# Kernel tuning notes

Hardware: AMD Instinct MI355X
Metric: run time of the kernel (lower is better)

The kernel has to match this reference:

```python
import jax, jax.numpy as jnp
import numpy as np

D_MODEL = 512
D_STATE = 64
D_CONV = 4
D_INNER = 1024   # expand=2 * d_model (mamba_ssm default)
DT_RANK = 32     # ceil(d_model/16)
NUM_CLASSES = 8
B, T, P, F = 8, 250, 20, 24   # x: [B, T*P=5000, F=24]
FLAT = T * P * F              # 120000 = fc1 input dim


def _mamba(u, in_proj_w, conv_w, conv_b, x_proj_w, dt_proj_w, dt_proj_b, A_log, D, out_proj_w):
    # u: [b, L, d_model]
    b, L, _ = u.shape
    xz = jnp.einsum('bld,ed->ble', u, in_proj_w)      # [b, L, 2*d_inner]
    x, z = jnp.split(xz, 2, axis=-1)                  # each [b, L, d_inner]
    # depthwise causal conv1d, kernel width D_CONV, truncated to L
    x_pad = jnp.pad(x, ((0, 0), (D_CONV - 1, 0), (0, 0)))
    x = sum(x_pad[:, k:k + L, :] * conv_w[:, k] for k in range(D_CONV)) + conv_b
    x = jax.nn.silu(x)
    x_dbl = jnp.einsum('bld,ed->ble', x, x_proj_w)    # [b, L, dt_rank + 2*d_state]
    dt, Bm, Cm = jnp.split(x_dbl, [DT_RANK, DT_RANK + D_STATE], axis=-1)
    dt = jax.nn.softplus(jnp.einsum('blr,dr->bld', dt, dt_proj_w) + dt_proj_b)  # [b, L, d_inner]
    A = -jnp.exp(A_log)                               # [d_inner, d_state]

    def step(h, inp):
        dt_t, B_t, C_t, u_t = inp                     # [b,d_in], [b,d_st], [b,d_st], [b,d_in]
        dA = jnp.exp(dt_t[:, :, None] * A)            # [b, d_in, d_st]
        dBu = dt_t[:, :, None] * B_t[:, None, :] * u_t[:, :, None]
        h = h * dA + dBu
        y = jnp.einsum('bds,bs->bd', h, C_t)
        return h, y

    xs = (jnp.swapaxes(dt, 0, 1), jnp.swapaxes(Bm, 0, 1), jnp.swapaxes(Cm, 0, 1), jnp.swapaxes(x, 0, 1))
    h0 = jnp.zeros((b, D_INNER, D_STATE), dtype=u.dtype)
    _, ys = jax.lax.scan(step, h0, xs)                # ys: [L, b, d_inner]
    y = jnp.swapaxes(ys, 0, 1) + x * D
    y = y * jax.nn.silu(z)
    return jnp.einsum('bld,ed->ble', y, out_proj_w)   # [b, L, d_model]


def setup_inputs() -> dict:
    key = jax.random.key(0)
    ks = jax.random.split(key, 16)
    n = lambda k, shape, s=0.02: jax.random.normal(k, shape, jnp.float32) * s
    return {
        'x': jax.random.normal(ks[0], (B, T * P, F), jnp.float32),
        'in_proj_w': n(ks[1], (2 * D_INNER, D_MODEL)),
        'conv_w': n(ks[2], (D_INNER, D_CONV), 0.1),
        'conv_b': jnp.zeros((D_INNER,), jnp.float32),
        'x_proj_w': n(ks[3], (DT_RANK + 2 * D_STATE, D_INNER)),
        'dt_proj_w': n(ks[4], (D_INNER, DT_RANK), 0.1),
        'dt_proj_b': jnp.full((D_INNER,), -4.6, jnp.float32),  # softplus -> dt ~ 0.01
        'A_log': jnp.log(jnp.broadcast_to(jnp.arange(1, D_STATE + 1, dtype=jnp.float32), (D_INNER, D_STATE))),
        'D': jnp.ones((D_INNER,), jnp.float32),
        'out_proj_w': n(ks[5], (D_MODEL, D_INNER)),
        'fc1_w': n(ks[6], (512, FLAT), 0.003),
        'fc1_b': jnp.zeros((512,), jnp.float32),
        'fc2_w': n(ks[7], (256, 512)),
        'fc2_b': jnp.zeros((256,), jnp.float32),
        'fc3_w': n(ks[8], (64, 256)),
        'fc3_b': jnp.zeros((64,), jnp.float32),
        'fc4_w': n(ks[9], (NUM_CLASSES, 64)),
        'fc4_b': jnp.zeros((NUM_CLASSES,), jnp.float32),
    }


def reference(x, in_proj_w, conv_w, conv_b, x_proj_w, dt_proj_w, dt_proj_b, A_log, D, out_proj_w,
              fc1_w, fc1_b, fc2_w, fc2_b, fc3_w, fc3_b, fc4_w, fc4_b):
    b = x.shape[0]
    u = x.reshape(b, T, P * F)                                   # [b,250,480]
    u = jnp.pad(u, ((0, 0), (0, 0), (0, D_MODEL - P * F)))       # pad 480 -> 512
    y = _mamba(u, in_proj_w, conv_w, conv_b, x_proj_w, dt_proj_w, dt_proj_b, A_log, D, out_proj_w)
    y = jax.nn.selu(y)                                           # AlphaDropout: identity in eval
    y = y[..., :P * F].reshape(b, T * P, F)                      # [b,5000,24]
    y = jnp.swapaxes(y, 1, 2).reshape(b, -1)                     # [b, 24*5000]
    y = y @ fc1_w.T + fc1_b
    y = y @ fc2_w.T + fc2_b
    y = y @ fc3_w.T + fc3_b
    return y @ fc4_w.T + fc4_b
```

## Files before the change

### kernel.cpp

```cpp
#include <hip/hip_runtime.h>
#include <math.h>

#define T_ 250
#define BL 2000
#define KIN 480
#define NFLAT 120000

typedef __attribute__((ext_vector_type(8))) short short8;
typedef __attribute__((ext_vector_type(4))) float f32x4;

__device__ __forceinline__ float sigmoidf_(float x){ return 1.0f/(1.0f+expf(-x)); }
__device__ __forceinline__ float siluf_(float x){ return x*sigmoidf_(x); }
__device__ __forceinline__ float softplusf_(float x){ return (x > 20.0f) ? x : log1pf(expf(x)); }
__device__ __forceinline__ float seluf_(float x){
  const float sc = 1.0507009873554804934193349852946f;
  const float al = 1.6732632423543772848170429916717f;
  return x > 0.0f ? sc*x : sc*al*expm1f(x);
}
__device__ __forceinline__ unsigned f2bf(float f){
  unsigned u = __builtin_bit_cast(unsigned, f);
  return (u + 0x7FFFu + ((u >> 16) & 1u)) >> 16;
}

template<int CTRL>
__device__ __forceinline__ float dpp_add(float x) {
  int t = __builtin_amdgcn_update_dpp(0, __builtin_bit_cast(int, x), CTRL, 0xF, 0xF, true);
  return x + __builtin_bit_cast(float, t);
}

__global__ __launch_bounds__(256) void inproj_mfma(
    const float* __restrict__ x, const float* __restrict__ w,
    float* __restrict__ C)
{
  __shared__ __align__(16) unsigned short As[128 * 40];
  __shared__ __align__(16) unsigned short Bs[128 * 40];
  const int tid = threadIdx.x;
  const int m0 = blockIdx.y * 128;
  const int n0 = blockIdx.x * 128;
  const int wid = tid >> 6, lane = tid & 63;
  const int wr = wid >> 1, wc = wid & 1;
  const int sr = tid >> 1;
  const int sk = (tid & 1) * 16;
  const int fr = lane & 15, fg = lane >> 4;

  float4 pa[4], pb[4];
  auto fetch = [&](int k0) {
    int m = m0 + sr;
    if (m < BL) {
      const float* xp = x + (size_t)m * KIN + k0 + sk;
      pa[0] = *(const float4*)(xp);
      pa[1] = *(const float4*)(xp + 4);
      pa[2] = *(const float4*)(xp + 8);
      pa[3] = *(const float4*)(xp + 12);
    } else {
      pa[0] = pa[1] = pa[2] = pa[3] = make_float4(0.f, 0.f, 0.f, 0.f);
    }
    const float* wp = w + (size_t)(n0 + sr) * 512 + k0 + sk;
    pb[0] = *(const float4*)(wp);
    pb[1] = *(const float4*)(wp + 4);
    pb[2] = *(const float4*)(wp + 8);
    pb[3] = *(const float4*)(wp + 12);
  };
  auto pack2 = [](float a, float b) {
    return f2bf(a) | (f2bf(b) << 16);
  };
  auto stash = [&](unsigned short* S, float4* p) {
    uint4 lo = make_uint4(pack2(p[0].x, p[0].y), pack2(p[0].z, p[0].w),
                          pack2(p[1].x, p[1].y), pack2(p[1].z, p[1].w));
    uint4 hi = make_uint4(pack2(p[2].x, p[2].y), pack2(p[2].z, p[2].w),
                          pack2(p[3].x, p[3].y), pack2(p[3].z, p[3].w));
    *(uint4*)&S[sr * 40 + sk] = lo;
    *(uint4*)&S[sr * 40 + sk + 8] = hi;
  };

  f32x4 acc[4][4];
#pragma unroll
  for (int i = 0; i < 4; ++i)
#pragma unroll
    for (int j = 0; j < 4; ++j) acc[i][j] = (f32x4)(0.0f);

  fetch(0);
  for (int k0 = 0; k0 < KIN; k0 += 32) {
    stash(As, pa);
    stash(Bs, pb);
    __syncthreads();
    if (k0 + 32 < KIN) fetch(k0 + 32);
    short8 av[4], bv[4];
#pragma unroll
    for (int fi = 0; fi < 4; ++fi)
      av[fi] = *(const short8*)&As[(wr * 64 + fi * 16 + fr) * 40 + fg * 8];
#pragma unroll
    for (int fj = 0; fj < 4; ++fj)
      bv[fj] = *(const short8*)&Bs[(wc * 64 + fj * 16 + fr) * 40 + fg * 8];
#pragma unroll
    for (int fi = 0; fi < 4; ++fi)
#pragma unroll
      for (int fj = 0; fj < 4; ++fj)
        acc[fi][fj] = __builtin_amdgcn_mfma_f32_16x16x32_bf16(
            av[fi], bv[fj], acc[fi][fj], 0, 0, 0);
    __syncthreads();
  }

#pragma unroll
  for (int fi = 0; fi < 4; ++fi) {
    int row = m0 + wr * 64 + fi * 16 + fg * 4;
#pragma unroll
    for (int fj = 0; fj < 4; ++fj) {
      int col = n0 + wc * 64 + fj * 16 + fr;
#pragma unroll
      for (int r = 0; r < 4; ++r)
        if (row + r < BL) C[(size_t)(row + r) * 2048 + col] = acc[fi][fj][r];
    }
  }
}

template<int EPI>
__global__ __launch_bounds__(256) void gemm_mfma64(
    const float* __restrict__ A, const float* __restrict__ W,
    float* __restrict__ C, int M, int N, int K, int lda, int ldb, int ldc)
{
  __shared__ __align__(16) unsigned short As[64 * 40];
  __shared__ __align__(16) unsigned short Bs[64 * 40];
  const int tid = threadIdx.x;
  const int m0 = blockIdx.y * 64;
  const int n0 = blockIdx.x * 64;
  const int kchunk = K / (int)gridDim.z;
  const int k_begin = blockIdx.z * kchunk;
  const int k_end = k_begin + kchunk;
  const int wid = tid >> 6, lane = tid & 63;
  const int wr = wid >> 1, wc = wid & 1;
  const int sr = tid >> 2;
  const int sk = (tid & 3) * 8;
  const int fr = lane & 15, fg = lane >> 4;

  float4 pa[2], pb[2];
  auto fetch = [&](int k0) {
    int m = m0 + sr;
    if (m < M) {
      const float* ap = A + (size_t)m * lda + k0 + sk;
      pa[0] = *(const float4*)(ap);
      pa[1] = *(const float4*)(ap + 4);
    } else {
      pa[0] = pa[1] = make_float4(0.f, 0.f, 0.f, 0.f);
    }
    int n = n0 + sr;
    if (n < N) {
      const float* wp = W + (size_t)n * ldb + k0 + sk;
      pb[0] = *(const float4*)(wp);
      pb[1] = *(const float4*)(wp + 4);
    } else {
      pb[0] = pb[1] = make_float4(0.f, 0.f, 0.f, 0.f);
    }
  };
  auto pack2 = [](float a, float b) {
    return f2bf(a) | (f2bf(b) << 16);
  };
  auto stash = [&](unsigned short* S, float4* p) {
    uint4 v = make_uint4(pack2(p[0].x, p[0].y), pack2(p[0].z, p[0].w),
                         pack2(p[1].x, p[1].y), pack2(p[1].z, p[1].w));
    *(uint4*)&S[sr * 40 + sk] = v;
  };

  f32x4 acc[2][2];
#pragma unroll
  for (int i = 0; i < 2; ++i)
#pragma unroll
    for (int j = 0; j < 2; ++j) acc[i][j] = (f32x4)(0.0f);

  fetch(k_begin);
  for (int k0 = k_begin; k0 < k_end; k0 += 32) {
    stash(As, pa);
    stash(Bs, pb);
    __syncthreads();
    if (k0 + 32 < k_end) fetch(k0 + 32);
    short8 av[2], bv[2];
#pragma unroll
    for (int fi = 0; fi < 2; ++fi)
      av[fi] = *(const short8*)&As[(wr * 32 + fi * 16 + fr) * 40 + fg * 8];
#pragma unroll
    for (int fj = 0; fj < 2; ++fj)
      bv[fj] = *(const short8*)&Bs[(wc * 32 + fj * 16 + fr) * 40 + fg * 8];
#pragma unroll
    for (int fi = 0; fi < 2; ++fi)
#pragma unroll
      for (int fj = 0; fj < 2; ++fj)
        acc[fi][fj] = __builtin_amdgcn_mfma_f32_16x16x32_bf16(
            av[fi], bv[fj], acc[fi][fj], 0, 0, 0);
    __syncthreads();
  }

#pragma unroll
  for (int fi = 0; fi < 2; ++fi) {
    int row0 = m0 + wr * 32 + fi * 16 + fg * 4;
#pragma unroll
    for (int fj = 0; fj < 2; ++fj) {
      int col = n0 + wc * 32 + fj * 16 + fr;
      if (col >= N) continue;
#pragma unroll
      for (int r = 0; r < 4; ++r) {
        int row = row0 + r;
        if (row >= M) continue;
        if constexpr (EPI == 0) {
          atomicAdd(&C[(size_t)row * ldc + col], acc[fi][fj][r]);
        } else {
          int b = row / 250, tt = row - b * 250;
          int p = col / 24, f = col - p * 24;
          C[(size_t)b * NFLAT + (size_t)f * 5000 + tt * 20 + p] =
              seluf_(acc[fi][fj][r]);
        }
      }
    }
  }
}

template<int BM, int BN, int BK, int TM, int TN>
__global__ __launch_bounds__(256, 2) void gemm_nt(
    const float* __restrict__ A, const float* __restrict__ W,
    float* __restrict__ C, const float* __restrict__ bias,
    int M, int N, int K, int lda, int ldb, int ldc, int epi)
{
  static_assert(BK == 32, "BK must be 32");
  __shared__ __align__(16) float As[BK][BM + 4];
  __shared__ __align__(16) float Bs[BK][BN + 4];
  constexpr int TNX = BN / TN;
  constexpr int TMX = BM / TM;
  static_assert(TNX * TMX == 256, "256 threads required");
  constexpr int AF4 = BM * BK / 1024;
  constexpr int BF4 = BN * BK / 1024;

  const int tid = threadIdx.x;
  const int tx = tid % TNX;
  const int ty = tid / TNX;
  const int m0 = blockIdx.y * BM;
  const int n0 = blockIdx.x * BN;
  const int kchunk = K / (int)gridDim.z;
  const int k_begin = blockIdx.z * kchunk;
  const int k_end = k_begin + kchunk;

  float4 pa[AF4], pb[BF4];

  auto fetch = [&](int k0) {
#pragma unroll
    for (int i = 0; i < AF4; ++i) {
      int fi = tid + 256 * i;
      int r = fi >> 3;
      int kc = (fi & 7) * 4;
      int m = m0 + r;
      pa[i] = (m < M) ? *(const float4*)(A + (size_t)m * lda + k0 + kc)
                      : make_float4(0.f, 0.f, 0.f, 0.f);
    }
#pragma unroll
    for (int i = 0; i < BF4; ++i) {
      int fi = tid + 256 * i;
      int r = fi >> 3;
      int kc = (fi & 7) * 4;
      int n = n0 + r;
      pb[i] = (n < N) ? *(const float4*)(W + (size_t)n * ldb + k0 + kc)
                      : make_float4(0.f, 0.f, 0.f, 0.f);
    }
  };

  fetch(k_begin);

  float acc[TM][TN];
#pragma unroll
  for (int i = 0; i < TM; ++i)
#pragma unroll
    for (int j = 0; j < TN; ++j) acc[i][j] = 0.0f;

  for (int k0 = k_begin; k0 < k_end; k0 += BK) {
#pragma unroll
    for (int i = 0; i < AF4; ++i) {
      int fi = tid + 256 * i;
      int r = fi >> 3;
      int kc = (fi & 7) * 4;
      As[kc + 0][r] = pa[i].x; As[kc + 1][r] = pa[i].y;
      As[kc + 2][r] = pa[i].z; As[kc + 3][r] = pa[i].w;
    }
#pragma unroll
    for (int i = 0; i < BF4; ++i) {
      int fi = tid + 256 * i;
      int r = fi >> 3;
      int kc = (fi & 7) * 4;
      Bs[kc + 0][r] = pb[i].x; Bs[kc + 1][r] = pb[i].y;
      Bs[kc + 2][r] = pb[i].z; Bs[kc + 3][r] = pb[i].w;
    }
    __syncthreads();
    if (k0 + BK < k_end) fetch(k0 + BK);
#pragma unroll
    for (int kk = 0; kk < BK; ++kk) {
      float a[TM], bb[TN];
      if constexpr ((TM & 3) == 0) {
#pragma unroll
        for (int t = 0; t < TM / 4; ++t) {
          float4 v = *(const float4*)&As[kk][ty * TM + t * 4];
          a[t*4+0] = v.x; a[t*4+1] = v.y; a[t*4+2] = v.z; a[t*4+3] = v.w;
        }
      } else {
#pragma unroll
        for (int i = 0; i < TM; ++i) a[i] = As[kk][ty * TM + i];
      }
      if constexpr ((TN & 3) == 0) {
#pragma unroll
        for (int t = 0; t < TN / 4; ++t) {
          float4 v = *(const float4*)&Bs[kk][tx * TN + t * 4];
          bb[t*4+0] = v.x; bb[t*4+1] = v.y; bb[t*4+2] = v.z; bb[t*4+3] = v.w;
        }
      } else {
#pragma unroll
        for (int j = 0; j < TN; ++j) bb[j] = Bs[kk][tx * TN + j];
      }
#pragma unroll
      for (int i = 0; i < TM; ++i)
#pragma unroll
        for (int j = 0; j < TN; ++j) acc[i][j] = fmaf(a[i], bb[j], acc[i][j]);
    }
    __syncthreads();
  }

#pragma unroll
  for (int i = 0; i < TM; ++i) {
    int m = m0 + ty * TM + i;
    if (m >= M) continue;
    if constexpr ((TN & 3) == 0) {
#pragma unroll
      for (int j0 = 0; j0 < TN; j0 += 4) {
        int n = n0 + tx * TN + j0;
        float v[4];
#pragma unroll
        for (int t = 0; t < 4; ++t) {
          float xv = acc[i][j0 + t];
          if (epi == 1) xv = softplusf_(xv + bias[n + t]);
          else if (epi == 2) xv = seluf_(xv);
          v[t] = xv;
        }
        if (epi == 3) {
#pragma unroll
          for (int t = 0; t < 4; ++t)
            if (n + t < N) atomicAdd(&C[(size_t)m * ldc + n + t], v[t]);
        } else if (n + 3 < N) {
          *(float4*)&C[(size_t)m * ldc + n] = make_float4(v[0], v[1], v[2], v[3]);
        } else {
#pragma unroll
          for (int t = 0; t < 4; ++t)
            if (n + t < N) C[(size_t)m * ldc + n + t] = v[t];
        }
      }
    } else {
#pragma unroll
      for (int j = 0; j < TN; ++j) {
        int n = n0 + tx * TN + j;
        if (n >= N) continue;
        float v = acc[i][j];
        if (epi == 1) v = softplusf_(v + bias[n]);
        else if (epi == 2) v = seluf_(v);
        if (epi == 3) atomicAdd(&C[(size_t)m * ldc + n], v);
        else C[(size_t)m * ldc + n] = v;
      }
    }
  }
}

__global__ __launch_bounds__(256) void conv_silu(
    float* __restrict__ xz, const float* __restrict__ cw,
    const float* __restrict__ cb, float* __restrict__ xc)
{
  int id = blockIdx.x * 256 + threadIdx.x;
  if (id >= BL * 256) return;
  int bl = id >> 8;
  int d4 = (id & 255) * 4;
  int l = bl % T_;
  float* base = xz + (size_t)bl * 2048 + d4;
  float4 x0 = *(const float4*)(base);
  float4 x1 = (l >= 1) ? *(const float4*)(base - 2048) : make_float4(0.f,0.f,0.f,0.f);
  float4 x2 = (l >= 2) ? *(const float4*)(base - 4096) : make_float4(0.f,0.f,0.f,0.f);
  float4 x3 = (l >= 3) ? *(const float4*)(base - 6144) : make_float4(0.f,0.f,0.f,0.f);
  float4 w0 = *(const float4*)(cw + (size_t)d4 * 4);
  float4 w1 = *(const float4*)(cw + (size_t)d4 * 4 + 4);
  float4 w2 = *(const float4*)(cw + (size_t)d4 * 4 + 8);
  float4 w3 = *(const float4*)(cw + (size_t)d4 * 4 + 12);
  float4 cbv = *(const float4*)(cb + d4);
  float4 o;
  o.x = siluf_(fmaf(x3.x, w0.x, fmaf(x2.x, w0.y, fmaf(x1.x, w0.z, fmaf(x0.x, w0.w, cbv.x)))));
  o.y = siluf_(fmaf(x3.y, w1.x, fmaf(x2.y, w1.y, fmaf(x1.y, w1.z, fmaf(x0.y, w1.w, cbv.y)))));
  o.z = siluf_(fmaf(x3.z, w2.x, fmaf(x2.z, w2.y, fmaf(x1.z, w2.z, fmaf(x0.z, w2.w, cbv.z)))));
  o.w = siluf_(fmaf(x3.w, w3.x, fmaf(x2.w, w3.y, fmaf(x1.w, w3.z, fmaf(x0.w, w3.w, cbv.w)))));
  *(float4*)(xc + (size_t)bl * 1024 + d4) = o;
  float4 zv = *(const float4*)(base + 1024);
  zv.x = siluf_(zv.x); zv.y = siluf_(zv.y); zv.z = siluf_(zv.z); zv.w = siluf_(zv.w);
  *(float4*)(base + 1024) = zv;
}

__global__ __launch_bounds__(256) void scan_kernel(
    const float* __restrict__ dtb, const float* __restrict__ xc,
    const float* __restrict__ xdbl, float* __restrict__ xz,
    const float* __restrict__ A_log, const float* __restrict__ Dp)
{
  int tid = threadIdx.x;
  int wv = tid >> 6, lane = tid & 63;
  int c = lane >> 5;
  int u = lane & 31;
  int w = blockIdx.x * 4 + wv;
  int b = w >> 9;
  int d = ((w & 511) << 1) + c;
  const float LOG2E = 1.4426950408889634f;
  float2 al = *(const float2*)(A_log + (size_t)d * 64 + u * 2);
  float am0 = -expf(al.x) * LOG2E;
  float am1 = -expf(al.y) * LOG2E;
  float Dv = Dp[d];
  float h0 = 0.f, h1 = 0.f;
  const float* dtp = dtb + (size_t)b * 256000 + d;
  const float* xp  = xc  + (size_t)b * 256000 + d;
  const float* zp  = xz  + (size_t)b * 512000 + 1024 + d;
  float*       yp  = xz  + (size_t)b * 512000 + d;
  const float* bp  = xdbl + (size_t)b * 40000 + 32 + u * 2;
  const float* cp  = bp + 64;

  float dt_f[4], xv_f[4], sz_f[4];
  float2 B_f[4], C_f[4];
#pragma unroll
  for (int i = 0; i < 4; ++i) {
    dt_f[i] = dtp[(size_t)i * 1024];
    xv_f[i] = xp[(size_t)i * 1024];
    sz_f[i] = zp[(size_t)i * 2048];
    B_f[i] = *(const float2*)(bp + (size_t)i * 160);
    C_f[i] = *(const float2*)(cp + (size_t)i * 160);
  }
  const bool outlane = (u == 16);

#pragma unroll 4
  for (int l = 0; l < 252; ++l) {
    int slot = l & 3;
    float dt = dt_f[slot], xv = xv_f[slot], sz = sz_f[slot];
    float2 Bv = B_f[slot], Cv = C_f[slot];
    dt_f[slot] = dtp[(size_t)(l + 4) * 1024];
    xv_f[slot] = xp[(size_t)(l + 4) * 1024];
    sz_f[slot] = zp[(size_t)(l + 4) * 2048];
    B_f[slot]  = *(const float2*)(bp + (size_t)(l + 4) * 160);
    C_f[slot]  = *(const float2*)(cp + (size_t)(l + 4) * 160);

    float dtx = dt * xv;
    h0 = fmaf(h0, exp2f(dt * am0), dtx * Bv.x);
    h1 = fmaf(h1, exp2f(dt * am1), dtx * Bv.y);
    float p = fmaf(h1, Cv.y, h0 * Cv.x);
    p = dpp_add<0xB1>(p);
    p = dpp_add<0x4E>(p);
    p = dpp_add<0x124>(p);
    p = dpp_add<0x128>(p);
    p = dpp_add<0x142>(p);
    if (outlane && l < T_) yp[(size_t)l * 2048] = fmaf(xv, Dv, p) * sz;
  }
}

__global__ __launch_bounds__(256) void fc1_kernel(
    const float* __restrict__ yfl, const float* __restrict__ W,
    float* __restrict__ r1)
{
  int blk = blockIdx.x;
  int ks = blk % 24;
  int cg = blk / 24;
  int wv = threadIdx.x >> 6;
  int lane = threadIdx.x & 63;
  int c0 = cg * 16 + wv * 4;
  const float* W0 = W + (size_t)c0 * NFLAT;
  float acc[4][8];
#pragma unroll
  for (int cc = 0; cc < 4; ++cc)
#pragma unroll
    for (int b = 0; b < 8; ++b) acc[cc][b] = 0.0f;

  int kbase = ks * 5000;
  int kend = kbase + 5000;
  for (int k = kbase + lane * 4; k + 4 <= kend; k += 256) {
    float4 w0 = *(const float4*)(W0 + k);
    float4 w1 = *(const float4*)(W0 + NFLAT + k);
    float4 w2 = *(const float4*)(W0 + 2 * (size_t)NFLAT + k);
    float4 w3 = *(const float4*)(W0 + 3 * (size_t)NFLAT + k);
#pragma unroll
    for (int b = 0; b < 8; ++b) {
      float4 y = *(const float4*)(yfl + (size_t)b * NFLAT + k);
      acc[0][b] = fmaf(w0.x, y.x, fmaf(w0.y, y.y, fmaf(w0.z, y.z, fmaf(w0.w, y.w, acc[0][b]))));
      acc[1][b] = fmaf(w1.x, y.x, fmaf(w1.y, y.y, fmaf(w1.z, y.z, fmaf(w1.w, y.w, acc[1][b]))));
      acc[2][b] = fmaf(w2.x, y.x, fmaf(w2.y, y.y, fmaf(w2.z, y.z, fmaf(w2.w, y.w, acc[2][b]))));
      acc[3][b] = fmaf(w3.x, y.x, fmaf(w3.y, y.y, fmaf(w3.z, y.z, fmaf(w3.w, y.w, acc[3][b]))));
    }
  }
#pragma unroll
  for (int cc = 0; cc < 4; ++cc)
#pragma unroll
    for (int b = 0; b < 8; ++b) {
      float s = acc[cc][b];
      s += __shfl_xor(s, 1);
      s += __shfl_xor(s, 2);
      s += __shfl_xor(s, 4);
      s += __shfl_xor(s, 8);
      s += __shfl_xor(s, 16);
      s += __shfl_xor(s, 32);
      if (lane == 0) atomicAdd(&r1[b * 512 + c0 + cc], s);
    }
}

__global__ __launch_bounds__(256) void fc2_kernel(
    const float* __restrict__ r1, const float* __restrict__ b1,
    const float* __restrict__ W2, const float* __restrict__ b2,
    float* __restrict__ r2)
{
  int wid = blockIdx.x * 4 + (threadIdx.x >> 6);
  int lane = threadIdx.x & 63;
  int b = wid >> 8;
  int j = wid & 255;
  int off = lane * 8;
  float4 ya = *(const float4*)(r1 + b * 512 + off);
  float4 yb = *(const float4*)(r1 + b * 512 + off + 4);
  float4 ba = *(const float4*)(b1 + off);
  float4 bbv = *(const float4*)(b1 + off + 4);
  float4 wa = *(const float4*)(W2 + (size_t)j * 512 + off);
  float4 wb = *(const float4*)(W2 + (size_t)j * 512 + off + 4);
  float p = (ya.x + ba.x) * wa.x + (ya.y + ba.y) * wa.y +
            (ya.z + ba.z) * wa.z + (ya.w + ba.w) * wa.w +
            (yb.x + bbv.x) * wb.x + (yb.y + bbv.y) * wb.y +
            (yb.z + bbv.z) * wb.z + (yb.w + bbv.w) * wb.w;
  p += __shfl_xor(p, 1);
  p += __shfl_xor(p, 2);
  p += __shfl_xor(p, 4);
  p += __shfl_xor(p, 8);
  p += __shfl_xor(p, 16);
  p += __shfl_xor(p, 32);
  if (lane == 0) r2[b * 256 + j] = p + b2[j];
}

__global__ __launch_bounds__(256) void fc34_kernel(
    const float* __restrict__ r2, const float* __restrict__ W3,
    const float* __restrict__ b3, const float* __restrict__ W4,
    const float* __restrict__ b4, float* __restrict__ out)
{
  __shared__ float a3[512];
  int tid = threadIdx.x;
  for (int o = tid; o < 512; o += 256) {
    int b = o >> 6, j = o & 63;
    float s = b3[j];
    const float* rr = r2 + b * 256;
    const float* wr = W3 + j * 256;
    for (int c = 0; c < 256; c += 4) {
      float4 rv = *(const float4*)(rr + c);
      float4 wv = *(const float4*)(wr + c);
      s = fmaf(rv.x, wv.x, fmaf(rv.y, wv.y, fmaf(rv.z, wv.z, fmaf(rv.w, wv.w, s))));
    }
    a3[o] = s;
  }
  __syncthreads();
  if (tid < 64) {
    int b = tid >> 3, j = tid & 7;
    float s = b4[j];
    const float* ar = a3 + b * 64;
    const float* wr = W4 + j * 64;
    for (int c = 0; c < 64; ++c) s = fmaf(ar[c], wr[c], s);
    out[b * 8 + j] = s;
  }
}

extern "C" void kernel_launch(void* const* d_in, const int* in_sizes, int n_in,
                              void* d_out, int out_size, void* d_ws, size_t ws_size,
                              hipStream_t stream) {
  const float* x      = (const float*)d_in[0];
  const float* w_in   = (const float*)d_in[1];
  const float* conv_w = (const float*)d_in[2];
  const float* conv_b = (const float*)d_in[3];
  const float* w_xp   = (const float*)d_in[4];
  const float* w_dt   = (const float*)d_in[5];
  const float* b_dt   = (const float*)d_in[6];
  const float* A_log  = (const float*)d_in[7];
  const float* Dp     = (const float*)d_in[8];
  const float* w_out  = (const float*)d_in[9];
  const float* w1 = (const float*)d_in[10];
  const float* b1 = (const float*)d_in[11];
  const float* w2 = (const float*)d_in[12];
  const float* b2 = (const float*)d_in[13];
  const float* w3 = (const float*)d_in[14];
  const float* b3 = (const float*)d_in[15];
  const float* w4 = (const float*)d_in[16];
  const float* b4 = (const float*)d_in[17];
  float* out = (float*)d_out;

  float* ws   = (float*)d_ws;
  float* xz   = ws;
  float* xc   = xz + 4096000;
  float* dtb  = xc + 2048000;
  float* ym   = dtb + 2048000;
  float* yfl  = ym + 960000;
  float* xdbl = yfl + 960000;
  float* r1   = xdbl + 320000;
  float* r2   = r1 + 4096;
  (void)ym;

  hipMemsetAsync(xdbl, 0, (320000 + 4096) * sizeof(float), stream);

  inproj_mfma<<<dim3(2048 / 128, 16, 1), 256, 0, stream>>>(x, w_in, xz);

  conv_silu<<<(BL * 256) / 256, 256, 0, stream>>>(xz, conv_w, conv_b, xc);

  gemm_mfma64<0><<<dim3(3, 32, 2), 256, 0, stream>>>(
      xc, w_xp, xdbl, BL, 160, 1024, 1024, 1024, 160);

  gemm_nt<32, 64, 32, 1, 8><<<dim3(1024 / 64, (BL + 31) / 32, 1), 256, 0, stream>>>(
      xdbl, w_dt, dtb, b_dt, BL, 1024, 32, 160, 32, 1024, 1);

  scan_kernel<<<1024, 256, 0, stream>>>(dtb, xc, xdbl, xz, A_log, Dp);

  gemm_mfma64<1><<<dim3(8, 32, 1), 256, 0, stream>>>(
      xz, w_out, yfl, BL, 480, 1024, 2048, 1024, 0);

  fc1_kernel<<<768, 256, 0, stream>>>(yfl, w1, r1);

  fc2_kernel<<<512, 256, 0, stream>>>(r1, b1, w2, b2, r2);

  fc34_kernel<<<1, 256, 0, stream>>>(r2, w3, b3, w4, b4, out);
}
```

Measured before the change: 614.5 us.

## Move dt_proj to MFMA GEMM, shrink in_proj tiles, raise x_proj split-K

The dt_proj GEMM now runs on the bf16 MFMA 64x64 kernel with a fused softplus+bias epilogue, replacing the scalar fp32 gemm_nt kernel, which is deleted. The in_proj tile shrinks from 128x128 to 128x64 so twice as many blocks are launched, and x_proj split-K goes from 2 to 4. These aim to use the matrix cores and fill more CUs on these small GEMMs. The cost is bf16 rounding on the dt path and more atomics for x_proj.

```diff
diff --git a/kernel.cpp b/kernel.cpp
--- a/kernel.cpp
+++ b/kernel.cpp
@@ -33,21 +33,23 @@
     float* __restrict__ C)
 {
   __shared__ __align__(16) unsigned short As[128 * 40];
-  __shared__ __align__(16) unsigned short Bs[128 * 40];
+  __shared__ __align__(16) unsigned short Bs[64 * 40];
   const int tid = threadIdx.x;
   const int m0 = blockIdx.y * 128;
-  const int n0 = blockIdx.x * 128;
+  const int n0 = blockIdx.x * 64;
   const int wid = tid >> 6, lane = tid & 63;
-  const int wr = wid >> 1, wc = wid & 1;
-  const int sr = tid >> 1;
-  const int sk = (tid & 1) * 16;
+  const int wr = wid;
+  const int sra = tid >> 1;
+  const int ska = (tid & 1) * 16;
+  const int srb = tid >> 2;
+  const int skb = (tid & 3) * 8;
   const int fr = lane & 15, fg = lane >> 4;
 
-  float4 pa[4], pb[4];
+  float4 pa[4], pb[2];
   auto fetch = [&](int k0) {
-    int m = m0 + sr;
+    int m = m0 + sra;
     if (m < BL) {
-      const float* xp = x + (size_t)m * KIN + k0 + sk;
+      const float* xp = x + (size_t)m * KIN + k0 + ska;
       pa[0] = *(const float4*)(xp);
       pa[1] = *(const float4*)(xp + 4);
       pa[2] = *(const float4*)(xp + 8);
@@ -55,45 +57,44 @@
     } else {
       pa[0] = pa[1] = pa[2] = pa[3] = make_float4(0.f, 0.f, 0.f, 0.f);
     }
-    const float* wp = w + (size_t)(n0 + sr) * 512 + k0 + sk;
+    const float* wp = w + (size_t)(n0 + srb) * 512 + k0 + skb;
     pb[0] = *(const float4*)(wp);
     pb[1] = *(const float4*)(wp + 4);
-    pb[2] = *(const float4*)(wp + 8);
-    pb[3] = *(const float4*)(wp + 12);
   };
   auto pack2 = [](float a, float b) {
     return f2bf(a) | (f2bf(b) << 16);
   };
-  auto stash = [&](unsigned short* S, float4* p) {
-    uint4 lo = make_uint4(pack2(p[0].x, p[0].y), pack2(p[0].z, p[0].w),
-                          pack2(p[1].x, p[1].y), pack2(p[1].z, p[1].w));
-    uint4 hi = make_uint4(pack2(p[2].x, p[2].y), pack2(p[2].z, p[2].w),
-                          pack2(p[3].x, p[3].y), pack2(p[3].z, p[3].w));
-    *(uint4*)&S[sr * 40 + sk] = lo;
-    *(uint4*)&S[sr * 40 + sk + 8] = hi;
-  };
-
-  f32x4 acc[4][4];
-#pragma unroll
-  for (int i = 0; i < 4; ++i)
+
+  f32x4 acc[2][4];
+#pragma unroll
+  for (int i = 0; i < 2; ++i)
 #pragma unroll
     for (int j = 0; j < 4; ++j) acc[i][j] = (f32x4)(0.0f);
 
   fetch(0);
   for (int k0 = 0; k0 < KIN; k0 += 32) {
-    stash(As, pa);
-    stash(Bs, pb);
+    {
+      uint4 lo = make_uint4(pack2(pa[0].x, pa[0].y), pack2(pa[0].z, pa[0].w),
+                            pack2(pa[1].x, pa[1].y), pack2(pa[1].z, pa[1].w));
+      uint4 hi = make_uint4(pack2(pa[2].x, pa[2].y), pack2(pa[2].z, pa[2].w),
+                            pack2(pa[3].x, pa[3].y), pack2(pa[3].z, pa[3].w));
+      *(uint4*)&As[sra * 40 + ska] = lo;
+      *(uint4*)&As[sra * 40 + ska + 8] = hi;
+      uint4 bb = make_uint4(pack2(pb[0].x, pb[0].y), pack2(pb[0].z, pb[0].w),
+                            pack2(pb[1].x, pb[1].y), pack2(pb[1].z, pb[1].w));
+      *(uint4*)&Bs[srb * 40 + skb] = bb;
+    }
     __syncthreads();
     if (k0 + 32 < KIN) fetch(k0 + 32);
-    short8 av[4], bv[4];
-#pragma unroll
-    for (int fi = 0; fi < 4; ++fi)
-      av[fi] = *(const short8*)&As[(wr * 64 + fi * 16 + fr) * 40 + fg * 8];
+    short8 av[2], bv[4];
+#pragma unroll
+    for (int fi = 0; fi < 2; ++fi)
+      av[fi] = *(const short8*)&As[(wr * 32 + fi * 16 + fr) * 40 + fg * 8];
 #pragma unroll
     for (int fj = 0; fj < 4; ++fj)
-      bv[fj] = *(const short8*)&Bs[(wc * 64 + fj * 16 + fr) * 40 + fg * 8];
-#pragma unroll
-    for (int fi = 0; fi < 4; ++fi)
+      bv[fj] = *(const short8*)&Bs[(fj * 16 + fr) * 40 + fg * 8];
+#pragma unroll
+    for (int fi = 0; fi < 2; ++fi)
 #pragma unroll
       for (int fj = 0; fj < 4; ++fj)
         acc[fi][fj] = __builtin_amdgcn_mfma_f32_16x16x32_bf16(
@@ -102,11 +103,11 @@
   }
 
 #pragma unroll
-  for (int fi = 0; fi < 4; ++fi) {
-    int row = m0 + wr * 64 + fi * 16 + fg * 4;
+  for (int fi = 0; fi < 2; ++fi) {
+    int row = m0 + wr * 32 + fi * 16 + fg * 4;
 #pragma unroll
     for (int fj = 0; fj < 4; ++fj) {
-      int col = n0 + wc * 64 + fj * 16 + fr;
+      int col = n0 + fj * 16 + fr;
 #pragma unroll
       for (int r = 0; r < 4; ++r)
         if (row + r < BL) C[(size_t)(row + r) * 2048 + col] = acc[fi][fj][r];
@@ -117,7 +118,8 @@
 template<int EPI>
 __global__ __launch_bounds__(256) void gemm_mfma64(
     const float* __restrict__ A, const float* __restrict__ W,
-    float* __restrict__ C, int M, int N, int K, int lda, int ldb, int ldc)
+    float* __restrict__ C, const float* __restrict__ bias,
+    int M, int N, int K, int lda, int ldb, int ldc)
 {
   __shared__ __align__(16) unsigned short As[64 * 40];
   __shared__ __align__(16) unsigned short Bs[64 * 40];
@@ -202,160 +204,14 @@
         if (row >= M) continue;
         if constexpr (EPI == 0) {
           atomicAdd(&C[(size_t)row * ldc + col], acc[fi][fj][r]);
-        } else {
+        } else if constexpr (EPI == 1) {
           int b = row / 250, tt = row - b * 250;
           int p = col / 24, f = col - p * 24;
           C[(size_t)b * NFLAT + (size_t)f * 5000 + tt * 20 + p] =
               seluf_(acc[fi][fj][r]);
+        } else {
+          C[(size_t)row * ldc + col] = softplusf_(acc[fi][fj][r] + bias[col]);
         }
-      }
-    }
-  }
-}
-
-template<int BM, int BN, int BK, int TM, int TN>
-__global__ __launch_bounds__(256, 2) void gemm_nt(
-    const float* __restrict__ A, const float* __restrict__ W,
-    float* __restrict__ C, const float* __restrict__ bias,
-    int M, int N, int K, int lda, int ldb, int ldc, int epi)
-{
-  static_assert(BK == 32, "BK must be 32");
-  __shared__ __align__(16) float As[BK][BM + 4];
-  __shared__ __align__(16) float Bs[BK][BN + 4];
-  constexpr int TNX = BN / TN;
-  constexpr int TMX = BM / TM;
-  static_assert(TNX * TMX == 256, "256 threads required");
-  constexpr int AF4 = BM * BK / 1024;
-  constexpr int BF4 = BN * BK / 1024;
-
-  const int tid = threadIdx.x;
-  const int tx = tid % TNX;
-  const int ty = tid / TNX;
-  const int m0 = blockIdx.y * BM;
-  const int n0 = blockIdx.x * BN;
-  const int kchunk = K / (int)gridDim.z;
-  const int k_begin = blockIdx.z * kchunk;
-  const int k_end = k_begin + kchunk;
-
-  float4 pa[AF4], pb[BF4];
-
-  auto fetch = [&](int k0) {
-#pragma unroll
-    for (int i = 0; i < AF4; ++i) {
-      int fi = tid + 256 * i;
-      int r = fi >> 3;
-      int kc = (fi & 7) * 4;
-      int m = m0 + r;
-      pa[i] = (m < M) ? *(const float4*)(A + (size_t)m * lda + k0 + kc)
-                      : make_float4(0.f, 0.f, 0.f, 0.f);
-    }
-#pragma unroll
-    for (int i = 0; i < BF4; ++i) {
-      int fi = tid + 256 * i;
-      int r = fi >> 3;
-      int kc = (fi & 7) * 4;
-      int n = n0 + r;
-      pb[i] = (n < N) ? *(const float4*)(W + (size_t)n * ldb + k0 + kc)
-                      : make_float4(0.f, 0.f, 0.f, 0.f);
-    }
-  };
-
-  fetch(k_begin);
-
-  float acc[TM][TN];
-#pragma unroll
-  for (int i = 0; i < TM; ++i)
-#pragma unroll
-    for (int j = 0; j < TN; ++j) acc[i][j] = 0.0f;
-
-  for (int k0 = k_begin; k0 < k_end; k0 += BK) {
-#pragma unroll
-    for (int i = 0; i < AF4; ++i) {
-      int fi = tid + 256 * i;
-      int r = fi >> 3;
-      int kc = (fi & 7) * 4;
-      As[kc + 0][r] = pa[i].x; As[kc + 1][r] = pa[i].y;
-      As[kc + 2][r] = pa[i].z; As[kc + 3][r] = pa[i].w;
-    }
-#pragma unroll
-    for (int i = 0; i < BF4; ++i) {
-      int fi = tid + 256 * i;
-      int r = fi >> 3;
-      int kc = (fi & 7) * 4;
-      Bs[kc + 0][r] = pb[i].x; Bs[kc + 1][r] = pb[i].y;
-      Bs[kc + 2][r] = pb[i].z; Bs[kc + 3][r] = pb[i].w;
-    }
-    __syncthreads();
-    if (k0 + BK < k_end) fetch(k0 + BK);
-#pragma unroll
-    for (int kk = 0; kk < BK; ++kk) {
-      float a[TM], bb[TN];
-      if constexpr ((TM & 3) == 0) {
-#pragma unroll
-        for (int t = 0; t < TM / 4; ++t) {
-          float4 v = *(const float4*)&As[kk][ty * TM + t * 4];
-          a[t*4+0] = v.x; a[t*4+1] = v.y; a[t*4+2] = v.z; a[t*4+3] = v.w;
-        }
-      } else {
-#pragma unroll
-        for (int i = 0; i < TM; ++i) a[i] = As[kk][ty * TM + i];
-      }
-      if constexpr ((TN & 3) == 0) {
-#pragma unroll
-        for (int t = 0; t < TN / 4; ++t) {
-          float4 v = *(const float4*)&Bs[kk][tx * TN + t * 4];
-          bb[t*4+0] = v.x; bb[t*4+1] = v.y; bb[t*4+2] = v.z; bb[t*4+3] = v.w;
-        }
-      } else {
-#pragma unroll
-        for (int j = 0; j < TN; ++j) bb[j] = Bs[kk][tx * TN + j];
-      }
-#pragma unroll
-      for (int i = 0; i < TM; ++i)
-#pragma unroll
-        for (int j = 0; j < TN; ++j) acc[i][j] = fmaf(a[i], bb[j], acc[i][j]);
-    }
-    __syncthreads();
-  }
-
-#pragma unroll
-  for (int i = 0; i < TM; ++i) {
-    int m = m0 + ty * TM + i;
-    if (m >= M) continue;
-    if constexpr ((TN & 3) == 0) {
-#pragma unroll
-      for (int j0 = 0; j0 < TN; j0 += 4) {
-        int n = n0 + tx * TN + j0;
-        float v[4];
-#pragma unroll
-        for (int t = 0; t < 4; ++t) {
-          float xv = acc[i][j0 + t];
-          if (epi == 1) xv = softplusf_(xv + bias[n + t]);
-          else if (epi == 2) xv = seluf_(xv);
-          v[t] = xv;
-        }
-        if (epi == 3) {
-#pragma unroll
-          for (int t = 0; t < 4; ++t)
-            if (n + t < N) atomicAdd(&C[(size_t)m * ldc + n + t], v[t]);
-        } else if (n + 3 < N) {
-          *(float4*)&C[(size_t)m * ldc + n] = make_float4(v[0], v[1], v[2], v[3]);
-        } else {
-#pragma unroll
-          for (int t = 0; t < 4; ++t)
-            if (n + t < N) C[(size_t)m * ldc + n + t] = v[t];
-        }
-      }
-    } else {
-#pragma unroll
-      for (int j = 0; j < TN; ++j) {
-        int n = n0 + tx * TN + j;
-        if (n >= N) continue;
-        float v = acc[i][j];
-        if (epi == 1) v = softplusf_(v + bias[n]);
-        else if (epi == 2) v = seluf_(v);
-        if (epi == 3) atomicAdd(&C[(size_t)m * ldc + n], v);
-        else C[(size_t)m * ldc + n] = v;
       }
     }
   }
@@ -595,20 +451,20 @@
 
   hipMemsetAsync(xdbl, 0, (320000 + 4096) * sizeof(float), stream);
 
-  inproj_mfma<<<dim3(2048 / 128, 16, 1), 256, 0, stream>>>(x, w_in, xz);
+  inproj_mfma<<<dim3(2048 / 64, 16, 1), 256, 0, stream>>>(x, w_in, xz);
 
   conv_silu<<<(BL * 256) / 256, 256, 0, stream>>>(xz, conv_w, conv_b, xc);
 
-  gemm_mfma64<0><<<dim3(3, 32, 2), 256, 0, stream>>>(
-      xc, w_xp, xdbl, BL, 160, 1024, 1024, 1024, 160);
-
-  gemm_nt<32, 64, 32, 1, 8><<<dim3(1024 / 64, (BL + 31) / 32, 1), 256, 0, stream>>>(
-      xdbl, w_dt, dtb, b_dt, BL, 1024, 32, 160, 32, 1024, 1);
+  gemm_mfma64<0><<<dim3(3, 32, 4), 256, 0, stream>>>(
+      xc, w_xp, xdbl, nullptr, BL, 160, 1024, 1024, 1024, 160);
+
+  gemm_mfma64<2><<<dim3(1024 / 64, 32, 1), 256, 0, stream>>>(
+      xdbl, w_dt, dtb, b_dt, BL, 1024, 32, 160, 32, 1024);
 
   scan_kernel<<<1024, 256, 0, stream>>>(dtb, xc, xdbl, xz, A_log, Dp);
 
   gemm_mfma64<1><<<dim3(8, 32, 1), 256, 0, stream>>>(
-      xz, w_out, yfl, BL, 480, 1024, 2048, 1024, 0);
+      xz, w_out, yfl, nullptr, BL, 480, 1024, 2048, 1024, 0);
 
   fc1_kernel<<<768, 256, 0, stream>>>(yfl, w1, r1);
 
```

Measured after the change: 609.5 us. About the same (-0.8%).
